# Performance work log

Measured on AMD Instinct MI355X. Metric: run time of the kernel, lower is better.

Reference implementation:

```python
import jax, jax.numpy as jnp
import numpy as np

B, T, D, H, E, K = 2, 1024, 1024, 16, 8, 2
HS = D // H
FF = 4 * D


def layernorm(x, g, b, eps=1e-5):
    m = jnp.mean(x, axis=-1, keepdims=True)
    v = jnp.mean((x - m) ** 2, axis=-1, keepdims=True)
    return (x - m) * jax.lax.rsqrt(v + eps) * g + b


def setup_inputs() -> dict:
    key = jax.random.key(0)
    ks = jax.random.split(key, 10)
    s = 0.02
    return {
        "x": jax.random.normal(ks[0], (B, T, D), jnp.float32),
        "Wq": jax.random.normal(ks[1], (H, D, HS), jnp.float32) * s,
        "Wk": jax.random.normal(ks[2], (H, D, HS), jnp.float32) * s,
        "Wv": jax.random.normal(ks[3], (H, D, HS), jnp.float32) * s,
        "gate_W": jax.random.normal(ks[4], (D, E), jnp.float32) * s,
        "W1": jax.random.normal(ks[5], (E, D, FF), jnp.float32) * s,
        "b1": jnp.zeros((E, FF), jnp.float32),
        "W2": jax.random.normal(ks[6], (E, FF, D), jnp.float32) * s,
        "b2": jnp.zeros((E, D), jnp.float32),
        "ln1_g": jnp.ones((D,), jnp.float32),
        "ln1_b": jnp.zeros((D,), jnp.float32),
        "ln2_g": jnp.ones((D,), jnp.float32),
        "ln2_b": jnp.zeros((D,), jnp.float32),
    }


def reference(x, Wq, Wk, Wv, gate_W, W1, b1, W2, b2, ln1_g, ln1_b, ln2_g, ln2_b):
    b, t, d = x.shape
    # --- multi-head causal attention (note: original scales by n_embed**-0.5) ---
    q = jnp.einsum("btd,hdf->bhtf", x, Wq)
    k = jnp.einsum("btd,hdf->bhtf", x, Wk)
    v = jnp.einsum("btd,hdf->bhtf", x, Wv)
    wei = jnp.einsum("bhtf,bhsf->bhts", q, k) * (d ** -0.5)
    mask = jnp.tril(jnp.ones((t, t), bool))
    wei = jnp.where(mask, wei, -jnp.inf)
    wei = jax.nn.softmax(wei, axis=-1)
    attn = jnp.einsum("bhts,bhsf->bhtf", wei, v)
    attn = attn.transpose(0, 2, 1, 3).reshape(b, t, d)  # concat heads

    y = x + layernorm(attn, ln1_g, ln1_b)

    # --- MoE: top-k gate, softmax over selected logits, weighted combine ---
    flat = y.reshape(-1, d)                         # [N, D]
    logits = flat @ gate_W                          # [N, E]
    topv, topi = jax.lax.top_k(logits, K)           # [N, K]
    w = jax.nn.softmax(topv, axis=-1)               # [N, K]
    combine = jnp.sum(jax.nn.one_hot(topi, E, dtype=flat.dtype) * w[..., None], axis=1)  # [N, E]

    h = jax.nn.relu(jnp.einsum("nd,edf->enf", flat, W1) + b1[:, None, :])  # [E, N, FF]
    eo = jnp.einsum("enf,efd->end", h, W2) + b2[:, None, :]                # [E, N, D]
    moe = jnp.einsum("ne,end->nd", combine, eo)                            # [N, D]

    out = y + layernorm(moe.reshape(b, t, d), ln2_g, ln2_b)
    return out
```

## Files before the change

### kernel.cpp

```cpp
#include <hip/hip_runtime.h>
#include <hip/hip_bf16.h>
#include <math.h>

typedef short short8 __attribute__((ext_vector_type(8)));
typedef float floatx4 __attribute__((ext_vector_type(4)));
typedef unsigned int u32_g __attribute__((address_space(1)));
typedef unsigned int u32_l __attribute__((address_space(3)));

__device__ __forceinline__ void gl_lds16(const void* g, void* l) {
    __builtin_amdgcn_global_load_lds((const u32_g*)g, (u32_l*)l, 16, 0, 0);
}

#define NB 2
#define TSEQ 1024
#define DIM 1024
#define NHEAD 16
#define HS 64
#define NEXP 8
#define FF 4096
#define NTOK (NB*TSEQ)
#define MAXSLOT 5120

#define OFF_Q      ((size_t)0)
#define OFF_K      ((size_t)8388608)
#define OFF_V      ((size_t)16777216)
#define OFF_ATTN   ((size_t)25165824)
#define OFF_Y      ((size_t)33554432)
#define OFF_YBF    ((size_t)41943040)
#define OFF_W1T    ((size_t)46137344)
#define OFF_MOE    ((size_t)113246208)
#define OFF_TOPKE  ((size_t)121634816)
#define OFF_TOPKW  ((size_t)121651200)
#define OFF_CNT    ((size_t)121667584)
#define OFF_PO     ((size_t)121667648)
#define OFF_CUR    ((size_t)121667712)
#define OFF_SLOTT  ((size_t)121667776)
#define OFF_SLOTW  ((size_t)121688256)
#define OFF_S      ((size_t)121708800)
#define OFF_XHI    (OFF_S)
#define OFF_XLO    (OFF_S + 4194304)
#define OFF_WTHI   (OFF_S + 8388608)
#define OFF_WTLO   (OFF_S + 14680064)
#define OFF_W2T    (OFF_S)
#define OFF_H      (OFF_S + 67108864)

#define OFF_ATTNB  (OFF_Q)

__global__ __launch_bounds__(256) void xsplit_kernel(
    const float* __restrict__ x, __hip_bfloat16* __restrict__ xhi, __hip_bfloat16* __restrict__ xlo)
{
    int idx = (blockIdx.x * 256 + threadIdx.x) * 4;
    float4 v = *(const float4*)(x + idx);
    float vv[4] = {v.x, v.y, v.z, v.w};
    union { ushort u[4]; ushort4 q; } hi, lo;
    #pragma unroll
    for (int l = 0; l < 4; ++l) {
        __hip_bfloat16 hb = __float2bfloat16(vv[l]);
        hi.u[l] = *(const ushort*)&hb;
        float r = vv[l] - __bfloat162float(hb);
        __hip_bfloat16 lb = __float2bfloat16(r);
        lo.u[l] = *(const ushort*)&lb;
    }
    *(ushort4*)((ushort*)xhi + idx) = hi.q;
    *(ushort4*)((ushort*)xlo + idx) = lo.q;
}

__global__ __launch_bounds__(256) void wsplit_kernel(
    const float* __restrict__ Wq, const float* __restrict__ Wk, const float* __restrict__ Wv,
    __hip_bfloat16* __restrict__ Wthi, __hip_bfloat16* __restrict__ Wtlo)
{
    int z = blockIdx.z, mat = z >> 4, hh = z & 15;
    const float* W = (mat == 0) ? Wq : ((mat == 1) ? Wk : Wv);
    const float* slab = W + (size_t)hh * DIM * HS;
    ushort* ohi = (ushort*)Wthi + (size_t)mat * (DIM * DIM) + (size_t)hh * HS * DIM;
    ushort* olo = (ushort*)Wtlo + (size_t)mat * (DIM * DIM) + (size_t)hh * HS * DIM;
    int c0 = blockIdx.x * 32, r0 = blockIdx.y * 32;
    __shared__ float tile[32][33];
    int t = threadIdx.x, i = t >> 3, j4 = (t & 7) * 4;
    float4 v4 = *(const float4*)(slab + (size_t)(r0 + i) * HS + c0 + j4);
    tile[i][j4] = v4.x; tile[i][j4+1] = v4.y; tile[i][j4+2] = v4.z; tile[i][j4+3] = v4.w;
    __syncthreads();
    union { ushort u[4]; ushort4 q; } hi, lo;
    #pragma unroll
    for (int l = 0; l < 4; ++l) {
        float xv = tile[j4 + l][i];
        __hip_bfloat16 hb = __float2bfloat16(xv);
        hi.u[l] = *(const ushort*)&hb;
        float r = xv - __bfloat162float(hb);
        __hip_bfloat16 lb = __float2bfloat16(r);
        lo.u[l] = *(const ushort*)&lb;
    }
    *(ushort4*)(ohi + (size_t)(c0 + i) * DIM + r0 + j4) = hi.q;
    *(ushort4*)(olo + (size_t)(c0 + i) * DIM + r0 + j4) = lo.q;
}

__global__ __launch_bounds__(256) void qkv_mfma(
    const __hip_bfloat16* __restrict__ xhi, const __hip_bfloat16* __restrict__ xlo,
    const __hip_bfloat16* __restrict__ Wthi, const __hip_bfloat16* __restrict__ Wtlo,
    float* __restrict__ Q, float* __restrict__ Kb, float* __restrict__ V)
{
    int mat = blockIdx.z;
    const __hip_bfloat16* Bhg = Wthi + (size_t)mat * (DIM * DIM);
    const __hip_bfloat16* Blg = Wtlo + (size_t)mat * (DIM * DIM);
    float* O = (mat == 0) ? Q : ((mat == 1) ? Kb : V);
    int n0 = blockIdx.x * 64, m0 = blockIdx.y * 128;
    int t = threadIdx.x, wave = t >> 6, lane = t & 63;
    __shared__ __hip_bfloat16 Ah[128][32];
    __shared__ __hip_bfloat16 Al[128][32];
    __shared__ __hip_bfloat16 Bh[64][32];
    __shared__ __hip_bfloat16 Bl[64][32];
    const __hip_bfloat16 *gAh[2], *gAl[2];
    __hip_bfloat16 *lAh[2], *lAl[2];
    #pragma unroll
    for (int p = 0; p < 2; ++p) {
        int lin = p * 256 + t, row = lin >> 2, seg = lin & 3;
        gAh[p] = xhi + (size_t)(m0 + row) * DIM + seg * 8;
        gAl[p] = xlo + (size_t)(m0 + row) * DIM + seg * 8;
        int cb = p * 256 + wave * 64;
        lAh[p] = &Ah[0][0] + (size_t)cb * 8;
        lAl[p] = &Al[0][0] + (size_t)cb * 8;
    }
    const __hip_bfloat16* gBh = Bhg + (size_t)(n0 + (t >> 2)) * DIM + (t & 3) * 8;
    const __hip_bfloat16* gBl = Blg + (size_t)(n0 + (t >> 2)) * DIM + (t & 3) * 8;
    __hip_bfloat16* lBh = &Bh[0][0] + (size_t)(wave * 64) * 8;
    __hip_bfloat16* lBl = &Bl[0][0] + (size_t)(wave * 64) * 8;

    int wr = (wave >> 1) * 64, wcl = (wave & 1) * 32;
    int lrow = lane & 15, quad = lane >> 4;
    floatx4 acc[4][2];
    #pragma unroll
    for (int i = 0; i < 4; ++i)
        #pragma unroll
        for (int j = 0; j < 2; ++j) acc[i][j] = (floatx4){0.f, 0.f, 0.f, 0.f};

    for (int k0 = 0; k0 < DIM; k0 += 32) {
        __syncthreads();
        gl_lds16(gAh[0] + k0, lAh[0]); gl_lds16(gAh[1] + k0, lAh[1]);
        gl_lds16(gAl[0] + k0, lAl[0]); gl_lds16(gAl[1] + k0, lAl[1]);
        gl_lds16(gBh + k0, lBh);       gl_lds16(gBl + k0, lBl);
        __syncthreads();
        short8 ah[4], al[4], bh[2], bl[2];
        #pragma unroll
        for (int i = 0; i < 4; ++i) {
            ah[i] = *(const short8*)(&Ah[wr + i * 16 + lrow][quad * 8]);
            al[i] = *(const short8*)(&Al[wr + i * 16 + lrow][quad * 8]);
        }
        #pragma unroll
        for (int j = 0; j < 2; ++j) {
            bh[j] = *(const short8*)(&Bh[wcl + j * 16 + lrow][quad * 8]);
            bl[j] = *(const short8*)(&Bl[wcl + j * 16 + lrow][quad * 8]);
        }
        #pragma unroll
        for (int i = 0; i < 4; ++i)
            #pragma unroll
            for (int j = 0; j < 2; ++j) {
                acc[i][j] = __builtin_amdgcn_mfma_f32_16x16x32_bf16(ah[i], bh[j], acc[i][j], 0, 0, 0);
                acc[i][j] = __builtin_amdgcn_mfma_f32_16x16x32_bf16(ah[i], bl[j], acc[i][j], 0, 0, 0);
                acc[i][j] = __builtin_amdgcn_mfma_f32_16x16x32_bf16(al[i], bh[j], acc[i][j], 0, 0, 0);
            }
    }
    #pragma unroll
    for (int i = 0; i < 4; ++i)
        #pragma unroll
        for (int j = 0; j < 2; ++j) {
            int ng = n0 + wcl + j * 16 + lrow;
            int hh = ng >> 6, f = ng & 63;
            #pragma unroll
            for (int r = 0; r < 4; ++r) {
                int mg = m0 + wr + i * 16 + quad * 4 + r;
                int bb = mg >> 10, tt = mg & 1023;
                O[(((size_t)bb * NHEAD + hh) * TSEQ + tt) * HS + f] = acc[i][j][r];
            }
        }
}

__global__ __launch_bounds__(256) void scores_kernel(
    const float* __restrict__ Q, const float* __restrict__ Kb, float* __restrict__ S)
{
    int tri = blockIdx.x, bh = blockIdx.y;
    int mt = 0; while (((mt + 1) * (mt + 2)) / 2 <= tri) ++mt;
    int nt = tri - (mt * (mt + 1)) / 2;
    int m0 = mt * 128, n0 = nt * 128;
    const float* Qb = Q + (size_t)bh * TSEQ * HS;
    const float* Kh = Kb + (size_t)bh * TSEQ * HS;
    float* Sb = S + (size_t)bh * TSEQ * TSEQ;
    __shared__ float As[16][132];
    __shared__ float Bs[16][132];
    int t = threadIdx.x, tx = t & 15, ty = t >> 4;
    float acc[8][8] = {{0.f}};
    for (int k0 = 0; k0 < HS; k0 += 16) {
        #pragma unroll
        for (int pss = 0; pss < 2; ++pss) {
            int lin = pss * 256 + t, m = lin >> 2, c = lin & 3;
            float4 v4 = *(const float4*)(Qb + (size_t)(m0 + m) * HS + k0 + c * 4);
            As[c*4+0][m] = v4.x; As[c*4+1][m] = v4.y; As[c*4+2][m] = v4.z; As[c*4+3][m] = v4.w;
        }
        #pragma unroll
        for (int pss = 0; pss < 2; ++pss) {
            int lin = pss * 256 + t, s = lin >> 2, c = lin & 3;
            float4 v4 = *(const float4*)(Kh + (size_t)(n0 + s) * HS + k0 + c * 4);
            Bs[c*4+0][s] = v4.x; Bs[c*4+1][s] = v4.y; Bs[c*4+2][s] = v4.z; Bs[c*4+3][s] = v4.w;
        }
        __syncthreads();
        #pragma unroll
        for (int kk = 0; kk < 16; ++kk) {
            float a[8], b[8];
            *(float4*)a       = *(const float4*)(&As[kk][ty * 4]);
            *(float4*)(a + 4) = *(const float4*)(&As[kk][64 + ty * 4]);
            *(float4*)b       = *(const float4*)(&Bs[kk][tx * 4]);
            *(float4*)(b + 4) = *(const float4*)(&Bs[kk][64 + tx * 4]);
            #pragma unroll
            for (int i = 0; i < 8; ++i)
                #pragma unroll
                for (int j = 0; j < 8; ++j) acc[i][j] += a[i] * b[j];
        }
        __syncthreads();
    }
    const float scale = 0.03125f;
    #pragma unroll
    for (int i = 0; i < 8; ++i) {
        int r = m0 + ((i < 4) ? ty * 4 + i : 64 + ty * 4 + (i - 4));
        #pragma unroll
        for (int jg = 0; jg < 2; ++jg) {
            int cb = n0 + ((jg == 0) ? tx * 4 : 64 + tx * 4);
            float4 v4 = make_float4(acc[i][jg*4+0]*scale, acc[i][jg*4+1]*scale,
                                    acc[i][jg*4+2]*scale, acc[i][jg*4+3]*scale);
            *(float4*)(Sb + (size_t)r * TSEQ + cb) = v4;
        }
    }
}

__global__ __launch_bounds__(256) void softmax_kernel(float* __restrict__ S)
{
    int row = blockIdx.x, bh = row >> 10, r = row & 1023;
    float* p = S + ((size_t)bh * TSEQ + r) * TSEQ;
    int len = r + 1, t = threadIdx.x;
    int klim = (r & ~127) + 128;
    float v[4]; float mx = -1e30f;
    #pragma unroll
    for (int i = 0; i < 4; ++i) { int c = t + i * 256; v[i] = (c < len) ? p[c] : -1e30f; mx = fmaxf(mx, v[i]); }
    __shared__ float redA[4];
    #pragma unroll
    for (int off = 32; off; off >>= 1) mx = fmaxf(mx, __shfl_down(mx, off));
    if ((t & 63) == 0) redA[t >> 6] = mx;
    __syncthreads();
    mx = fmaxf(fmaxf(redA[0], redA[1]), fmaxf(redA[2], redA[3]));
    float sum = 0.f;
    #pragma unroll
    for (int i = 0; i < 4; ++i) { int c = t + i * 256; float e = (c < len) ? expf(v[i] - mx) : 0.f; v[i] = e; sum += e; }
    __shared__ float redB[4];
    #pragma unroll
    for (int off = 32; off; off >>= 1) sum += __shfl_down(sum, off);
    if ((t & 63) == 0) redB[t >> 6] = sum;
    __syncthreads();
    float inv = 1.f / (redB[0] + redB[1] + redB[2] + redB[3]);
    #pragma unroll
    for (int i = 0; i < 4; ++i) { int c = t + i * 256; if (c < klim) p[c] = v[i] * inv; }
}

__global__ __launch_bounds__(256) void pv_kernel(
    const float* __restrict__ S, const float* __restrict__ V,
    float* __restrict__ attn, float* __restrict__ attnB)
{
    int mt = blockIdx.x, bh = blockIdx.y, z = blockIdx.z;
    int m0 = mt * 128;
    int half = (m0 >> 1) + 64;
    int kbeg = z ? half : 0;
    int kend = z ? (m0 + 128) : half;
    float* O = z ? attnB : attn;
    const float* P = S + (size_t)bh * TSEQ * TSEQ;
    const float* Vb = V + (size_t)bh * TSEQ * HS;
    __shared__ float As[16][132];
    __shared__ float Bs[16][68];
    int t = threadIdx.x, tx = t & 15, ty = t >> 4;
    float acc[8][4] = {{0.f}};
    for (int k0 = kbeg; k0 < kend; k0 += 16) {
        #pragma unroll
        for (int pss = 0; pss < 2; ++pss) {
            int lin = pss * 256 + t, m = lin >> 2, c = lin & 3;
            float4 v4 = *(const float4*)(P + (size_t)(m0 + m) * TSEQ + k0 + c * 4);
            As[c*4+0][m] = v4.x; As[c*4+1][m] = v4.y; As[c*4+2][m] = v4.z; As[c*4+3][m] = v4.w;
        }
        { int kk = t >> 4, c = t & 15;
          float4 v4 = *(const float4*)(Vb + (size_t)(k0 + kk) * HS + c * 4);
          *(float4*)(&Bs[kk][c * 4]) = v4; }
        __syncthreads();
        #pragma unroll
        for (int kk = 0; kk < 16; ++kk) {
            float a[8], b[4];
            *(float4*)a       = *(const float4*)(&As[kk][ty * 4]);
            *(float4*)(a + 4) = *(const float4*)(&As[kk][64 + ty * 4]);
            *(float4*)b       = *(const float4*)(&Bs[kk][tx * 4]);
            #pragma unroll
            for (int i = 0; i < 8; ++i)
                #pragma unroll
                for (int j = 0; j < 4; ++j) acc[i][j] += a[i] * b[j];
        }
        __syncthreads();
    }
    int b = bh >> 4, hh = bh & 15;
    #pragma unroll
    for (int i = 0; i < 8; ++i) {
        int r = m0 + ((i < 4) ? ty * 4 + i : 64 + ty * 4 + (i - 4));
        float4 v4 = make_float4(acc[i][0], acc[i][1], acc[i][2], acc[i][3]);
        *(float4*)(O + ((size_t)b * TSEQ + r) * DIM + hh * HS + tx * 4) = v4;
    }
}

__global__ __launch_bounds__(256) void ln1_kernel(
    const float* __restrict__ x, const float* __restrict__ attn, const float* __restrict__ attnB,
    const float* __restrict__ g, const float* __restrict__ bta,
    float* __restrict__ y, __hip_bfloat16* __restrict__ ybf)
{
    int n = blockIdx.x, t = threadIdx.x;
    const float* a = attn + (size_t)n * DIM;
    const float* aB = attnB + (size_t)n * DIM;
    float v[4]; float s = 0.f;
    #pragma unroll
    for (int i = 0; i < 4; ++i) { int c = t + i * 256; v[i] = a[c] + aB[c]; s += v[i]; }
    __shared__ float redA[4];
    #pragma unroll
    for (int off = 32; off; off >>= 1) s += __shfl_down(s, off);
    if ((t & 63) == 0) redA[t >> 6] = s;
    __syncthreads();
    float mean = (redA[0] + redA[1] + redA[2] + redA[3]) * (1.f / 1024.f);
    float s2 = 0.f;
    #pragma unroll
    for (int i = 0; i < 4; ++i) { float d = v[i] - mean; s2 += d * d; }
    __shared__ float redB[4];
    #pragma unroll
    for (int off = 32; off; off >>= 1) s2 += __shfl_down(s2, off);
    if ((t & 63) == 0) redB[t >> 6] = s2;
    __syncthreads();
    float rstd = rsqrtf((redB[0] + redB[1] + redB[2] + redB[3]) * (1.f / 1024.f) + 1e-5f);
    #pragma unroll
    for (int i = 0; i < 4; ++i) {
        int d = t + i * 256;
        float val = x[(size_t)n * DIM + d] + (v[i] - mean) * rstd * g[d] + bta[d];
        y[(size_t)n * DIM + d] = val;
        ybf[(size_t)n * DIM + d] = __float2bfloat16(val);
    }
}

__global__ __launch_bounds__(256) void transpose_kernel(
    const float* __restrict__ in, __hip_bfloat16* __restrict__ out, int R, int C)
{
    const float* ie = in + (size_t)blockIdx.z * R * C;
    __hip_bfloat16* oe = out + (size_t)blockIdx.z * R * C;
    int c0 = blockIdx.x * 32, r0 = blockIdx.y * 32;
    __shared__ float tile[32][33];
    int t = threadIdx.x, i = t >> 3, j4 = (t & 7) * 4;
    float4 v4 = *(const float4*)(ie + (size_t)(r0 + i) * C + c0 + j4);
    tile[i][j4] = v4.x; tile[i][j4+1] = v4.y; tile[i][j4+2] = v4.z; tile[i][j4+3] = v4.w;
    __syncthreads();
    union { ushort u[4]; ushort4 v; } pk;
    #pragma unroll
    for (int l = 0; l < 4; ++l) {
        __hip_bfloat16 hb = __float2bfloat16(tile[j4 + l][i]);
        pk.u[l] = *(const ushort*)&hb;
    }
    *(ushort4*)((ushort*)oe + (size_t)(c0 + i) * R + r0 + j4) = pk.v;
}

__global__ __launch_bounds__(256) void gate_kernel(
    const float* __restrict__ y, const float* __restrict__ gW,
    int* __restrict__ topk_e, float* __restrict__ topk_w, int* __restrict__ cnt)
{
    int n = blockIdx.x, t = threadIdx.x;
    const float* yr = y + (size_t)n * DIM;
    float p[8] = {0.f,0.f,0.f,0.f,0.f,0.f,0.f,0.f};
    for (int d = t; d < DIM; d += 256) {
        float yv = yr[d];
        const float* w = gW + (size_t)d * NEXP;
        #pragma unroll
        for (int e = 0; e < 8; ++e) p[e] += yv * w[e];
    }
    #pragma unroll
    for (int e = 0; e < 8; ++e)
        #pragma unroll
        for (int off = 32; off; off >>= 1) p[e] += __shfl_down(p[e], off);
    __shared__ float lg[4][8];
    if ((t & 63) == 0) { int w = t >> 6;
        #pragma unroll
        for (int e = 0; e < 8; ++e) lg[w][e] = p[e]; }
    __syncthreads();
    if (t == 0) {
        float l[8];
        #pragma unroll
        for (int e = 0; e < 8; ++e) l[e] = lg[0][e] + lg[1][e] + lg[2][e] + lg[3][e];
        int e0 = 0; float v0 = l[0];
        for (int e = 1; e < 8; ++e) if (l[e] > v0) { v0 = l[e]; e0 = e; }
        int e1 = 0; float v1 = -1e30f;
        for (int e = 0; e < 8; ++e) if (e != e0 && l[e] > v1) { v1 = l[e]; e1 = e; }
        float z = expf(v1 - v0);
        float w0 = 1.f / (1.f + z), w1 = z / (1.f + z);
        topk_e[n * 2] = e0; topk_e[n * 2 + 1] = e1;
        topk_w[n * 2] = w0; topk_w[n * 2 + 1] = w1;
        atomicAdd(&cnt[e0], 1); atomicAdd(&cnt[e1], 1);
    }
}

__global__ void scan_kernel(const int* __restrict__ cnt, int* __restrict__ po, int* __restrict__ cursor)
{
    if (threadIdx.x == 0 && blockIdx.x == 0) {
        int acc = 0;
        for (int e = 0; e < 8; ++e) { po[e] = acc; cursor[e] = acc; acc += ((cnt[e] + 127) >> 7) << 7; }
        po[8] = acc;
    }
}

__global__ void scatter_kernel(const int* __restrict__ topk_e, const float* __restrict__ topk_w,
                               int* __restrict__ cursor, int* __restrict__ slot_token, float* __restrict__ slot_w)
{
    int i = blockIdx.x * 256 + threadIdx.x;
    int e = topk_e[i];
    int pos = atomicAdd(&cursor[e], 1);
    slot_token[pos] = i >> 1;
    slot_w[pos] = topk_w[i];
}

__global__ __launch_bounds__(256) void moe_gemm1(
    const __hip_bfloat16* __restrict__ ybf, const __hip_bfloat16* __restrict__ W1t,
    const float* __restrict__ b1, const int* __restrict__ po, const int* __restrict__ cnt,
    const int* __restrict__ slot_token, __hip_bfloat16* __restrict__ h)
{
    int flat = blockIdx.x;
    int xcd = flat & 7, j = flat >> 3;
    int n0 = (((j & 3) << 3) + xcd) * 128;
    int m0 = (j >> 2) * 128;
    int total = po[8];
    if (m0 >= total) return;
    int e = 0;
    for (int i = 0; i < 8; ++i) if (m0 >= po[i] && m0 < po[i + 1]) e = i;
    int valid = po[e] + cnt[e] - m0; if (valid > 128) valid = 128;
    int t = threadIdx.x, wave = t >> 6, lane = t & 63;
    __shared__ int tok[128];
    __shared__ __hip_bfloat16 As[128][64];
    __shared__ __hip_bfloat16 Bs[128][64];
    if (t < 128) tok[t] = (t < valid) ? slot_token[m0 + t] : slot_token[m0];
    __syncthreads();
    const __hip_bfloat16 *gA[4], *gB[4];
    __hip_bfloat16 *lA[4], *lB[4];
    #pragma unroll
    for (int p = 0; p < 4; ++p) {
        int lin = p * 256 + t, row = lin >> 3, seg = lin & 7;
        gA[p] = ybf + (size_t)tok[row] * DIM + seg * 8;
        gB[p] = W1t + ((size_t)e * FF + n0 + row) * DIM + seg * 8;
        int cb = p * 256 + wave * 64;
        lA[p] = &As[0][0] + (size_t)cb * 8;
        lB[p] = &Bs[0][0] + (size_t)cb * 8;
    }
    int wr = (wave >> 1) * 64, wc = (wave & 1) * 64;
    int lrow = lane & 15, quad = lane >> 4;
    floatx4 acc[4][4];
    #pragma unroll
    for (int i = 0; i < 4; ++i)
        #pragma unroll
        for (int j2 = 0; j2 < 4; ++j2) acc[i][j2] = (floatx4){0.f, 0.f, 0.f, 0.f};
    for (int k0 = 0; k0 < DIM; k0 += 64) {
        __syncthreads();
        #pragma unroll
        for (int p = 0; p < 4; ++p) { gl_lds16(gA[p] + k0, lA[p]); gl_lds16(gB[p] + k0, lB[p]); }
        __syncthreads();
        #pragma unroll
        for (int ks = 0; ks < 2; ++ks) {
            short8 a[4], b[4];
            #pragma unroll
            for (int i = 0; i < 4; ++i) a[i] = *(const short8*)(&As[wr + i * 16 + lrow][ks * 32 + quad * 8]);
            #pragma unroll
            for (int j2 = 0; j2 < 4; ++j2) b[j2] = *(const short8*)(&Bs[wc + j2 * 16 + lrow][ks * 32 + quad * 8]);
            #pragma unroll
            for (int i = 0; i < 4; ++i)
                #pragma unroll
                for (int j2 = 0; j2 < 4; ++j2)
                    acc[i][j2] = __builtin_amdgcn_mfma_f32_16x16x32_bf16(a[i], b[j2], acc[i][j2], 0, 0, 0);
        }
    }
    #pragma unroll
    for (int i = 0; i < 4; ++i)
        #pragma unroll
        for (int j2 = 0; j2 < 4; ++j2) {
            int col = n0 + wc + j2 * 16 + lrow;
            float bias = b1[e * FF + col];
            #pragma unroll
            for (int r = 0; r < 4; ++r) {
                int row = wr + i * 16 + quad * 4 + r;
                float vv = fmaxf(acc[i][j2][r] + bias, 0.f);
                h[(size_t)(m0 + row) * FF + col] = __float2bfloat16(vv);
            }
        }
}

__global__ __launch_bounds__(256) void moe_gemm2(
    const __hip_bfloat16* __restrict__ h, const __hip_bfloat16* __restrict__ W2t,
    const float* __restrict__ b2, const int* __restrict__ po, const int* __restrict__ cnt,
    const int* __restrict__ slot_token, const float* __restrict__ slot_w, float* __restrict__ moe)
{
    int flat = blockIdx.x;
    int xcd = flat & 7, j = flat >> 3;
    int n0 = xcd * 128;
    int kz = j & 1;
    int m0 = (j >> 1) * 128;
    int total = po[8];
    if (m0 >= total) return;
    int e = 0;
    for (int i = 0; i < 8; ++i) if (m0 >= po[i] && m0 < po[i + 1]) e = i;
    int valid = po[e] + cnt[e] - m0; if (valid > 128) valid = 128;
    int t = threadIdx.x, wave = t >> 6, lane = t & 63;
    __shared__ int tokS[128];
    __shared__ float wS[128];
    __shared__ __hip_bfloat16 As[128][64];
    __shared__ __hip_bfloat16 Bs[128][64];
    if (t < 128) {
        tokS[t] = (t < valid) ? slot_token[m0 + t] : 0;
        wS[t]   = (t < valid) ? slot_w[m0 + t] : 0.f;
    }
    __syncthreads();
    const __hip_bfloat16 *gA[4], *gB[4];
    __hip_bfloat16 *lA[4], *lB[4];
    #pragma unroll
    for (int p = 0; p < 4; ++p) {
        int lin = p * 256 + t, row = lin >> 3, seg = lin & 7;
        gA[p] = h + (size_t)(m0 + row) * FF + seg * 8;
        gB[p] = W2t + ((size_t)e * DIM + n0 + row) * FF + seg * 8;
        int cb = p * 256 + wave * 64;
        lA[p] = &As[0][0] + (size_t)cb * 8;
        lB[p] = &Bs[0][0] + (size_t)cb * 8;
    }
    int wr = (wave >> 1) * 64, wc = (wave & 1) * 64;
    int lrow = lane & 15, quad = lane >> 4;
    floatx4 acc[4][4];
    #pragma unroll
    for (int i = 0; i < 4; ++i)
        #pragma unroll
        for (int j2 = 0; j2 < 4; ++j2) acc[i][j2] = (floatx4){0.f, 0.f, 0.f, 0.f};
    int kbeg = kz * (FF / 2), kend = kbeg + (FF / 2);
    for (int k0 = kbeg; k0 < kend; k0 += 64) {
        __syncthreads();
        #pragma unroll
        for (int p = 0; p < 4; ++p) { gl_lds16(gA[p] + k0, lA[p]); gl_lds16(gB[p] + k0, lB[p]); }
        __syncthreads();
        #pragma unroll
        for (int ks = 0; ks < 2; ++ks) {
            short8 a[4], b[4];
            #pragma unroll
            for (int i = 0; i < 4; ++i) a[i] = *(const short8*)(&As[wr + i * 16 + lrow][ks * 32 + quad * 8]);
            #pragma unroll
            for (int j2 = 0; j2 < 4; ++j2) b[j2] = *(const short8*)(&Bs[wc + j2 * 16 + lrow][ks * 32 + quad * 8]);
            #pragma unroll
            for (int i = 0; i < 4; ++i)
                #pragma unroll
                for (int j2 = 0; j2 < 4; ++j2)
                    acc[i][j2] = __builtin_amdgcn_mfma_f32_16x16x32_bf16(a[i], b[j2], acc[i][j2], 0, 0, 0);
        }
    }
    #pragma unroll
    for (int i = 0; i < 4; ++i)
        #pragma unroll
        for (int j2 = 0; j2 < 4; ++j2) {
            int col = n0 + wc + j2 * 16 + lrow;
            float bias = (kz == 0) ? b2[e * DIM + col] : 0.f;
            #pragma unroll
            for (int r = 0; r < 4; ++r) {
                int row = wr + i * 16 + quad * 4 + r;
                if (row < valid) {
                    float vv = acc[i][j2][r] + bias;
                    atomicAdd(&moe[(size_t)tokS[row] * DIM + col], wS[row] * vv);
                }
            }
        }
}

__global__ __launch_bounds__(256) void ln2_kernel(
    const float* __restrict__ y, const float* __restrict__ moe,
    const float* __restrict__ g, const float* __restrict__ bta, float* __restrict__ out)
{
    int n = blockIdx.x, t = threadIdx.x;
    const float* a = moe + (size_t)n * DIM;
    float v[4]; float s = 0.f;
    #pragma unroll
    for (int i = 0; i < 4; ++i) { v[i] = a[t + i * 256]; s += v[i]; }
    __shared__ float redA[4];
    #pragma unroll
    for (int off = 32; off; off >>= 1) s += __shfl_down(s, off);
    if ((t & 63) == 0) redA[t >> 6] = s;
    __syncthreads();
    float mean = (redA[0] + redA[1] + redA[2] + redA[3]) * (1.f / 1024.f);
    float s2 = 0.f;
    #pragma unroll
    for (int i = 0; i < 4; ++i) { float d = v[i] - mean; s2 += d * d; }
    __shared__ float redB[4];
    #pragma unroll
    for (int off = 32; off; off >>= 1) s2 += __shfl_down(s2, off);
    if ((t & 63) == 0) redB[t >> 6] = s2;
    __syncthreads();
    float rstd = rsqrtf((redB[0] + redB[1] + redB[2] + redB[3]) * (1.f / 1024.f) + 1e-5f);
    #pragma unroll
    for (int i = 0; i < 4; ++i) {
        int d = t + i * 256;
        out[(size_t)n * DIM + d] = y[(size_t)n * DIM + d] + (v[i] - mean) * rstd * g[d] + bta[d];
    }
}

extern "C" void kernel_launch(void* const* d_in, const int* in_sizes, int n_in,
                              void* d_out, int out_size, void* d_ws, size_t ws_size,
                              hipStream_t stream)
{
    const float* x    = (const float*)d_in[0];
    const float* Wq   = (const float*)d_in[1];
    const float* Wk   = (const float*)d_in[2];
    const float* Wv   = (const float*)d_in[3];
    const float* gW   = (const float*)d_in[4];
    const float* W1   = (const float*)d_in[5];
    const float* b1   = (const float*)d_in[6];
    const float* W2   = (const float*)d_in[7];
    const float* b2   = (const float*)d_in[8];
    const float* ln1g = (const float*)d_in[9];
    const float* ln1b = (const float*)d_in[10];
    const float* ln2g = (const float*)d_in[11];
    const float* ln2b = (const float*)d_in[12];
    float* out = (float*)d_out;

    char* ws = (char*)d_ws;
    float* Q    = (float*)(ws + OFF_Q);
    float* Kb   = (float*)(ws + OFF_K);
    float* V    = (float*)(ws + OFF_V);
    float* attn = (float*)(ws + OFF_ATTN);
    float* attnB= (float*)(ws + OFF_ATTNB);
    float* y    = (float*)(ws + OFF_Y);
    __hip_bfloat16* ybf = (__hip_bfloat16*)(ws + OFF_YBF);
    __hip_bfloat16* W1t = (__hip_bfloat16*)(ws + OFF_W1T);
    float* moe  = (float*)(ws + OFF_MOE);
    int*   topk_e = (int*)(ws + OFF_TOPKE);
    float* topk_w = (float*)(ws + OFF_TOPKW);
    int*   cnt    = (int*)(ws + OFF_CNT);
    int*   po     = (int*)(ws + OFF_PO);
    int*   cur    = (int*)(ws + OFF_CUR);
    int*   slot_t = (int*)(ws + OFF_SLOTT);
    float* slot_w = (float*)(ws + OFF_SLOTW);
    float* S      = (float*)(ws + OFF_S);
    __hip_bfloat16* xhi  = (__hip_bfloat16*)(ws + OFF_XHI);
    __hip_bfloat16* xlo  = (__hip_bfloat16*)(ws + OFF_XLO);
    __hip_bfloat16* Wthi = (__hip_bfloat16*)(ws + OFF_WTHI);
    __hip_bfloat16* Wtlo = (__hip_bfloat16*)(ws + OFF_WTLO);
    __hip_bfloat16* W2t = (__hip_bfloat16*)(ws + OFF_W2T);
    __hip_bfloat16* h   = (__hip_bfloat16*)(ws + OFF_H);

    hipMemsetAsync(cnt, 0, 32, stream);
    hipMemsetAsync(moe, 0, (size_t)NTOK * DIM * 4, stream);

    xsplit_kernel<<<2048, 256, 0, stream>>>(x, xhi, xlo);
    wsplit_kernel<<<dim3(2, 32, 48), 256, 0, stream>>>(Wq, Wk, Wv, Wthi, Wtlo);
    qkv_mfma<<<dim3(16, 16, 3), 256, 0, stream>>>(xhi, xlo, Wthi, Wtlo, Q, Kb, V);
    scores_kernel<<<dim3(36, 32), 256, 0, stream>>>(Q, Kb, S);
    softmax_kernel<<<NB * NHEAD * TSEQ, 256, 0, stream>>>(S);
    pv_kernel<<<dim3(8, 32, 2), 256, 0, stream>>>(S, V, attn, attnB);
    ln1_kernel<<<NTOK, 256, 0, stream>>>(x, attn, attnB, ln1g, ln1b, y, ybf);
    gate_kernel<<<NTOK, 256, 0, stream>>>(y, gW, topk_e, topk_w, cnt);
    scan_kernel<<<1, 64, 0, stream>>>(cnt, po, cur);
    scatter_kernel<<<16, 256, 0, stream>>>(topk_e, topk_w, cur, slot_t, slot_w);
    transpose_kernel<<<dim3(128, 32, 8), 256, 0, stream>>>(W1, W1t, DIM, FF);
    moe_gemm1<<<1280, 256, 0, stream>>>(ybf, W1t, b1, po, cnt, slot_t, h);
    transpose_kernel<<<dim3(32, 128, 8), 256, 0, stream>>>(W2, W2t, FF, DIM);
    moe_gemm2<<<640, 256, 0, stream>>>(h, W2t, b2, po, cnt, slot_t, slot_w, moe);
    ln2_kernel<<<NTOK, 256, 0, stream>>>(y, moe, ln2g, ln2b, out);
}
```

Before: 836.3 us.

## Replace atomic MoE scatter-combine with slot-indexed gather in LN2

The second expert GEMM no longer scatters weighted results into a zeroed moe buffer with float atomics. Each split-K half now writes plain stores to its own per-slot buffer (eoA, eoB), and ln2 gathers each token's two slots, sums the halves and applies the gate weights. This removes the memset and the atomic contention, and makes the reduction deterministic. In exchange it writes and re-reads two full per-slot fp32 expert-output buffers, and it reuses the W1t and moe workspace regions.

```diff
diff --git a/kernel.cpp b/kernel.cpp
--- a/kernel.cpp
+++ b/kernel.cpp
@@ -45,6 +45,9 @@
 #define OFF_H      (OFF_S + 67108864)
 
 #define OFF_ATTNB  (OFF_Q)
+#define OFF_SLOTOF (OFF_MOE)
+#define OFF_EOA    (OFF_W1T)
+#define OFF_EOB    (OFF_W1T + 20971520)
 
 __global__ __launch_bounds__(256) void xsplit_kernel(
     const float* __restrict__ x, __hip_bfloat16* __restrict__ xhi, __hip_bfloat16* __restrict__ xlo)
@@ -410,13 +413,14 @@
 }
 
 __global__ void scatter_kernel(const int* __restrict__ topk_e, const float* __restrict__ topk_w,
-                               int* __restrict__ cursor, int* __restrict__ slot_token, float* __restrict__ slot_w)
+                               int* __restrict__ cursor, int* __restrict__ slot_token,
+                               int* __restrict__ slot_of)
 {
     int i = blockIdx.x * 256 + threadIdx.x;
     int e = topk_e[i];
     int pos = atomicAdd(&cursor[e], 1);
     slot_token[pos] = i >> 1;
-    slot_w[pos] = topk_w[i];
+    slot_of[i] = pos;
 }
 
 __global__ __launch_bounds__(256) void moe_gemm1(
@@ -493,8 +497,8 @@
 
 __global__ __launch_bounds__(256) void moe_gemm2(
     const __hip_bfloat16* __restrict__ h, const __hip_bfloat16* __restrict__ W2t,
-    const float* __restrict__ b2, const int* __restrict__ po, const int* __restrict__ cnt,
-    const int* __restrict__ slot_token, const float* __restrict__ slot_w, float* __restrict__ moe)
+    const float* __restrict__ b2, const int* __restrict__ po,
+    float* __restrict__ eoA, float* __restrict__ eoB)
 {
     int flat = blockIdx.x;
     int xcd = flat & 7, j = flat >> 3;
@@ -505,17 +509,9 @@
     if (m0 >= total) return;
     int e = 0;
     for (int i = 0; i < 8; ++i) if (m0 >= po[i] && m0 < po[i + 1]) e = i;
-    int valid = po[e] + cnt[e] - m0; if (valid > 128) valid = 128;
     int t = threadIdx.x, wave = t >> 6, lane = t & 63;
-    __shared__ int tokS[128];
-    __shared__ float wS[128];
     __shared__ __hip_bfloat16 As[128][64];
     __shared__ __hip_bfloat16 Bs[128][64];
-    if (t < 128) {
-        tokS[t] = (t < valid) ? slot_token[m0 + t] : 0;
-        wS[t]   = (t < valid) ? slot_w[m0 + t] : 0.f;
-    }
-    __syncthreads();
     const __hip_bfloat16 *gA[4], *gB[4];
     __hip_bfloat16 *lA[4], *lB[4];
     #pragma unroll
@@ -554,6 +550,7 @@
                     acc[i][j2] = __builtin_amdgcn_mfma_f32_16x16x32_bf16(a[i], b[j2], acc[i][j2], 0, 0, 0);
         }
     }
+    float* eo = kz ? eoB : eoA;
     #pragma unroll
     for (int i = 0; i < 4; ++i)
         #pragma unroll
@@ -563,23 +560,31 @@
             #pragma unroll
             for (int r = 0; r < 4; ++r) {
                 int row = wr + i * 16 + quad * 4 + r;
-                if (row < valid) {
-                    float vv = acc[i][j2][r] + bias;
-                    atomicAdd(&moe[(size_t)tokS[row] * DIM + col], wS[row] * vv);
-                }
+                eo[(size_t)(m0 + row) * DIM + col] = acc[i][j2][r] + bias;
             }
         }
 }
 
 __global__ __launch_bounds__(256) void ln2_kernel(
-    const float* __restrict__ y, const float* __restrict__ moe,
+    const float* __restrict__ y,
+    const float* __restrict__ eoA, const float* __restrict__ eoB,
+    const int* __restrict__ slot_of, const float* __restrict__ topk_w,
     const float* __restrict__ g, const float* __restrict__ bta, float* __restrict__ out)
 {
     int n = blockIdx.x, t = threadIdx.x;
-    const float* a = moe + (size_t)n * DIM;
+    int s0 = slot_of[n * 2], s1 = slot_of[n * 2 + 1];
+    float w0 = topk_w[n * 2], w1 = topk_w[n * 2 + 1];
+    const float* a0 = eoA + (size_t)s0 * DIM;
+    const float* b0 = eoB + (size_t)s0 * DIM;
+    const float* a1 = eoA + (size_t)s1 * DIM;
+    const float* b1r = eoB + (size_t)s1 * DIM;
     float v[4]; float s = 0.f;
     #pragma unroll
-    for (int i = 0; i < 4; ++i) { v[i] = a[t + i * 256]; s += v[i]; }
+    for (int i = 0; i < 4; ++i) {
+        int c = t + i * 256;
+        v[i] = w0 * (a0[c] + b0[c]) + w1 * (a1[c] + b1r[c]);
+        s += v[i];
+    }
     __shared__ float redA[4];
     #pragma unroll
     for (int off = 32; off; off >>= 1) s += __shfl_down(s, off);
@@ -630,14 +635,13 @@
     float* y    = (float*)(ws + OFF_Y);
     __hip_bfloat16* ybf = (__hip_bfloat16*)(ws + OFF_YBF);
     __hip_bfloat16* W1t = (__hip_bfloat16*)(ws + OFF_W1T);
-    float* moe  = (float*)(ws + OFF_MOE);
     int*   topk_e = (int*)(ws + OFF_TOPKE);
     float* topk_w = (float*)(ws + OFF_TOPKW);
     int*   cnt    = (int*)(ws + OFF_CNT);
     int*   po     = (int*)(ws + OFF_PO);
     int*   cur    = (int*)(ws + OFF_CUR);
     int*   slot_t = (int*)(ws + OFF_SLOTT);
-    float* slot_w = (float*)(ws + OFF_SLOTW);
+    int*   slot_of= (int*)(ws + OFF_SLOTOF);
     float* S      = (float*)(ws + OFF_S);
     __hip_bfloat16* xhi  = (__hip_bfloat16*)(ws + OFF_XHI);
     __hip_bfloat16* xlo  = (__hip_bfloat16*)(ws + OFF_XLO);
@@ -645,9 +649,10 @@
     __hip_bfloat16* Wtlo = (__hip_bfloat16*)(ws + OFF_WTLO);
     __hip_bfloat16* W2t = (__hip_bfloat16*)(ws + OFF_W2T);
     __hip_bfloat16* h   = (__hip_bfloat16*)(ws + OFF_H);
+    float* eoA = (float*)(ws + OFF_EOA);
+    float* eoB = (float*)(ws + OFF_EOB);
 
     hipMemsetAsync(cnt, 0, 32, stream);
-    hipMemsetAsync(moe, 0, (size_t)NTOK * DIM * 4, stream);
 
     xsplit_kernel<<<2048, 256, 0, stream>>>(x, xhi, xlo);
     wsplit_kernel<<<dim3(2, 32, 48), 256, 0, stream>>>(Wq, Wk, Wv, Wthi, Wtlo);
@@ -658,10 +663,10 @@
     ln1_kernel<<<NTOK, 256, 0, stream>>>(x, attn, attnB, ln1g, ln1b, y, ybf);
     gate_kernel<<<NTOK, 256, 0, stream>>>(y, gW, topk_e, topk_w, cnt);
     scan_kernel<<<1, 64, 0, stream>>>(cnt, po, cur);
-    scatter_kernel<<<16, 256, 0, stream>>>(topk_e, topk_w, cur, slot_t, slot_w);
+    scatter_kernel<<<16, 256, 0, stream>>>(topk_e, topk_w, cur, slot_t, slot_of);
     transpose_kernel<<<dim3(128, 32, 8), 256, 0, stream>>>(W1, W1t, DIM, FF);
     moe_gemm1<<<1280, 256, 0, stream>>>(ybf, W1t, b1, po, cnt, slot_t, h);
     transpose_kernel<<<dim3(32, 128, 8), 256, 0, stream>>>(W2, W2t, FF, DIM);
-    moe_gemm2<<<640, 256, 0, stream>>>(h, W2t, b2, po, cnt, slot_t, slot_w, moe);
-    ln2_kernel<<<NTOK, 256, 0, stream>>>(y, moe, ln2g, ln2b, out);
-}
+    moe_gemm2<<<640, 256, 0, stream>>>(h, W2t, b2, po, eoA, eoB);
+    ln2_kernel<<<NTOK, 256, 0, stream>>>(y, eoA, eoB, slot_of, topk_w, ln2g, ln2b, out);
+}
```

Measured after the change: 770.7 us. 7.8% less time.
